# Optimization experiments

Measured on AMD Instinct MI355X. Metric: run time of the kernel, lower is better.

Reference implementation:

```python
import jax, jax.numpy as jnp
import numpy as np

N_NODES = 100000
N_EDGES = 1600000
IN_CH = 128
HID = 128
EMBED = 256
NUM_GRAPHS = 128


def setup_inputs() -> dict:
    key = jax.random.key(0)
    ks = jax.random.split(key, 12)
    x = jax.random.normal(ks[0], (N_NODES, IN_CH), dtype=jnp.float32)
    edge_index = jax.random.randint(ks[1], (2, N_EDGES), 0, N_NODES, dtype=jnp.int64)
    batch = jnp.sort(jax.random.randint(ks[2], (N_NODES,), 0, NUM_GRAPHS, dtype=jnp.int64))
    s = 0.05
    # conv1 MLP: Linear(in_ch,128) -> ReLU -> Linear(128,128)
    W11 = jax.random.normal(ks[3], (IN_CH, HID), dtype=jnp.float32) * s
    b11 = jnp.zeros((HID,), dtype=jnp.float32)
    W12 = jax.random.normal(ks[4], (HID, HID), dtype=jnp.float32) * s
    b12 = jnp.zeros((HID,), dtype=jnp.float32)
    # conv2 MLP: Linear(128,128) -> ReLU -> Linear(128,embed)
    W21 = jax.random.normal(ks[5], (HID, HID), dtype=jnp.float32) * s
    b21 = jnp.zeros((HID,), dtype=jnp.float32)
    W22 = jax.random.normal(ks[6], (HID, EMBED), dtype=jnp.float32) * s
    b22 = jnp.zeros((EMBED,), dtype=jnp.float32)
    gamma = jnp.ones((EMBED,), dtype=jnp.float32)
    beta = jnp.zeros((EMBED,), dtype=jnp.float32)
    return {"x": x, "edge_index": edge_index, "batch": batch,
            "W11": W11, "b11": b11, "W12": W12, "b12": b12,
            "W21": W21, "b21": b21, "W22": W22, "b22": b22,
            "gamma": gamma, "beta": beta}


def _gin_conv(x, src, dst, W_a, b_a, W_b, b_b):
    # GINConv with eps=0: MLP(x + sum_{j in N(i)} x_j)
    msgs = x[src]                                   # [E, d] gather
    agg = jax.ops.segment_sum(msgs, dst, num_segments=N_NODES)  # scatter-add
    h = x + agg
    h = jax.nn.relu(h @ W_a + b_a)
    return h @ W_b + b_b


def reference(x, edge_index, batch, W11, b11, W12, b12, W21, b21, W22, b22, gamma, beta):
    src, dst = edge_index[0], edge_index[1]
    h = jax.nn.relu(_gin_conv(x, src, dst, W11, b11, W12, b12))   # [N, 128]
    h = jax.nn.relu(_gin_conv(h, src, dst, W21, b21, W22, b22))   # [N, 256]
    # global_mean_pool over graphs
    sums = jax.ops.segment_sum(h, batch, num_segments=NUM_GRAPHS)           # [G, 256]
    counts = jax.ops.segment_sum(jnp.ones((N_NODES,), h.dtype), batch, num_segments=NUM_GRAPHS)
    pooled = sums / jnp.maximum(counts, 1.0)[:, None]
    # LayerNorm over last dim (eps=1e-5 as in torch)
    mu = jnp.mean(pooled, axis=-1, keepdims=True)
    var = jnp.var(pooled, axis=-1, keepdims=True)
    out = (pooled - mu) * jax.lax.rsqrt(var + 1e-5) * gamma + beta
    # Dropout in eval mode: identity
    return out
```

## Files before the change

kernel.cpp:

```cpp
#include <hip/hip_runtime.h>

#define GRAPHS 128
#define CHUNKC 4000

typedef _Float16 f16x8 __attribute__((ext_vector_type(8)));
typedef _Float16 f16x4 __attribute__((ext_vector_type(4)));
typedef _Float16 f16x2 __attribute__((ext_vector_type(2)));
typedef float f32x4 __attribute__((ext_vector_type(4)));

__device__ __forceinline__ void fmix_lo(float& a, int w) {
  asm("v_fma_mix_f32 %0, %1, 1.0, %0 op_sel:[0,0,0] op_sel_hi:[1,0,0]" : "+v"(a) : "v"(w));
}
__device__ __forceinline__ void fmix_hi(float& a, int w) {
  asm("v_fma_mix_f32 %0, %1, 1.0, %0 op_sel:[1,0,0] op_sel_hi:[1,0,0]" : "+v"(a) : "v"(w));
}

__global__ void k_prep(const int* __restrict__ dst, int* __restrict__ histG,
                       int e, int NB, int NW,
                       const float* __restrict__ x, _Float16* __restrict__ P0,
                       _Float16* __restrict__ P1, int n,
                       const float* __restrict__ W11, const float* __restrict__ W12,
                       const float* __restrict__ W21, const float* __restrict__ W22,
                       f16x8* __restrict__ f11, f16x8* __restrict__ f12,
                       f16x8* __restrict__ f21, f16x8* __restrict__ f22,
                       float* __restrict__ pool, int cvtb, int wpb, int poolb) {
  __shared__ int h[256];
  int b = blockIdx.x, t = threadIdx.x;
  if (b < NW) {
    h[t] = 0; __syncthreads();
    int lo = b * CHUNKC, hi = min(lo + CHUNKC, e);
    for (int i = lo + t; i < hi; i += 256) atomicAdd(&h[dst[i] >> 9], 1);
    __syncthreads();
    if (t < NB) histG[t * NW + b] = h[t];
    return;
  }
  b -= NW;
  if (b < cvtb) {
    int i = b * 256 + t;
    if (i < n * 32) {
      float4 v = ((const float4*)x)[i];
      f16x4 hh = { (_Float16)v.x, (_Float16)v.y, (_Float16)v.z, (_Float16)v.w };
      ((f16x4*)P0)[i] = hh;
    }
    return;
  }
  b -= cvtb;
  if (b < wpb) {
    int id = b * 256 + t;
    const float* W; f16x8* F; int C, cid, fshift;
    if (id < 2048)       { W = W11; F = f11; C = 128; cid = id;        fshift = 3; }
    else if (id < 4096)  { W = W12; F = f12; C = 128; cid = id - 2048; fshift = 3; }
    else if (id < 6144)  { W = W21; F = f21; C = 128; cid = id - 4096; fshift = 3; }
    else if (id < 10240) { W = W22; F = f22; C = 256; cid = id - 6144; fshift = 4; }
    else return;
    int lane = cid & 63;
    int rest = cid >> 6;
    int fc = rest & ((1 << fshift) - 1);
    int kk = rest >> fshift;
    int cout = fc * 16 + (lane & 15);
    int kb = kk * 32 + (lane >> 4) * 8;
    f16x8 v;
#pragma unroll
    for (int q = 0; q < 8; ++q) v[q] = (_Float16)W[(size_t)(kb + q) * C + cout];
    F[cid] = v;
    return;
  }
  b -= wpb;
  if (b < poolb) {
    int i = b * 256 + t;
    if (i < GRAPHS * 256) pool[i] = 0.f;
    return;
  }
  if (t < 128) P0[(size_t)n * 128 + t] = (_Float16)0.f;
  else P1[(size_t)n * 128 + (t - 128)] = (_Float16)0.f;
}

__global__ void k_scanA(const int* __restrict__ in, int* __restrict__ out,
                        int* __restrict__ bsum, int N) {
  __shared__ int s[256];
  int t = threadIdx.x, b = blockIdx.x;
  int base = b * 1024 + t * 4;
  int v[4]; int tot = 0;
#pragma unroll
  for (int j = 0; j < 4; ++j) { int i = base + j; v[j] = (i < N) ? in[i] : 0; tot += v[j]; }
  s[t] = tot; __syncthreads();
  for (int o = 1; o < 256; o <<= 1) {
    int x = (t >= o) ? s[t - o] : 0;
    __syncthreads(); s[t] += x; __syncthreads();
  }
  int run = s[t] - tot;
#pragma unroll
  for (int j = 0; j < 4; ++j) { int i = base + j; if (i < N) out[i] = run; run += v[j]; }
  if (t == 255) bsum[b] = s[255];
}

__global__ void k_scanB(int* bsum, int nb, const int* __restrict__ batch,
                        int* __restrict__ starts, int n) {
  __shared__ int s[256];
  int t = threadIdx.x;
  int v = (t < nb) ? bsum[t] : 0;
  s[t] = v; __syncthreads();
  for (int o = 1; o < 256; o <<= 1) {
    int x = (t >= o) ? s[t - o] : 0;
    __syncthreads(); s[t] += x; __syncthreads();
  }
  if (t < nb) bsum[t] = s[t] - v;
  if (t <= GRAPHS) {
    int lo = 0, hi = n;
    while (lo < hi) { int mid = (lo + hi) >> 1; if (batch[mid] < t) lo = mid + 1; else hi = mid; }
    starts[t] = lo;
  }
}

__global__ void k_part(const int* __restrict__ src, const int* __restrict__ dst,
                       const int* __restrict__ histG, const int* __restrict__ off,
                       const int* __restrict__ bsum,
                       int* __restrict__ part, int e, int NB, int NW) {
  __shared__ int hist[256], lbA[256], lbB[256], stmp[256];
  __shared__ int els[CHUNKC];
  int t = threadIdx.x, w = blockIdx.x;
  int hv = (t < NB) ? histG[t * NW + w] : 0;
  hist[t] = hv; stmp[t] = hv; __syncthreads();
  for (int o = 1; o < 256; o <<= 1) {
    int x = (t >= o) ? stmp[t - o] : 0;
    __syncthreads(); stmp[t] += x; __syncthreads();
  }
  lbA[t] = stmp[t] - hv; lbB[t] = stmp[t] - hv;
  __syncthreads();
  int lo = w * CHUNKC, hi = min(lo + CHUNKC, e);
  for (int i = lo + t; i < hi; i += 256) {
    int d = dst[i];
    int p = atomicAdd(&lbB[d >> 9], 1);
    els[p] = src[i] | ((d & 511) << 17);
  }
  __syncthreads();
  int ln = t & 63, wv = t >> 6;
  for (int b = wv; b < NB; b += 4) {
    int c = hist[b], lb = lbA[b];
    int idx = b * NW + w;
    long g = off[idx] + bsum[idx >> 10];
    for (int j = ln; j < c; j += 64) part[g + j] = els[lb + j];
  }
}

__global__ void k_csrb(const int* __restrict__ part, const int* __restrict__ off,
                       const int* __restrict__ bsum,
                       int* __restrict__ ptr, int* __restrict__ csr,
                       int e, int NB, int NW, int n) {
  __shared__ int nh[512], ncur[512], stmp[256];
  int t = threadIdx.x, b = blockIdx.x;
  int i0 = b * NW;
  int s0 = off[i0] + bsum[i0 >> 10];
  int e0 = e;
  if (b + 1 < NB) { int i1 = (b + 1) * NW; e0 = off[i1] + bsum[i1 >> 10]; }
  nh[t] = 0; nh[t + 256] = 0; __syncthreads();
  for (int i = s0 + t; i < e0; i += 256) atomicAdd(&nh[((unsigned)part[i]) >> 17], 1);
  __syncthreads();
  int v0 = nh[2 * t], v1 = nh[2 * t + 1];
  int ps = v0 + v1;
  stmp[t] = ps; __syncthreads();
  for (int o = 1; o < 256; o <<= 1) {
    int x = (t >= o) ? stmp[t - o] : 0;
    __syncthreads(); stmp[t] += x; __syncthreads();
  }
  int base = stmp[t] - ps;
  __syncthreads();
  nh[2 * t] = base;   nh[2 * t + 1] = base + v0;
  ncur[2 * t] = base; ncur[2 * t + 1] = base + v0;
  __syncthreads();
#pragma unroll
  for (int q = 0; q < 2; ++q) {
    int vv = t + q * 256;
    int node = (b << 9) + vv;
    if (node <= n) ptr[node] = s0 + nh[vv];
  }
  for (int i = s0 + t; i < e0; i += 256) {
    int u = part[i];
    int p = atomicAdd(&ncur[((unsigned)u) >> 17], 1);
    csr[s0 + p] = u & 0x1FFFF;
  }
}

__global__ void k_agg_h(const _Float16* __restrict__ in, _Float16* __restrict__ out,
                        const int* __restrict__ ptr, const int* __restrict__ csr, int n) {
  int gid = blockIdx.x * 256 + threadIdx.x;
  int node = gid >> 6, lane = gid & 63;
  if (node >= n) return;
  const f16x8* inp = (const f16x8*)in;
  int cb = lane & 15, rg = lane >> 4;
  f16x8 self = inp[(size_t)node * 16 + cb];
  float acc[8];
#pragma unroll
  for (int c = 0; c < 8; ++c) acc[c] = (rg == 0) ? (float)self[c] : 0.f;
  int s = ptr[node], deg = ptr[node + 1] - s;
  union W { f16x8 v; int i[4]; };
  for (int seg = 0; seg < deg; seg += 64) {
    int my = (seg + lane < deg) ? csr[s + seg + lane] : n;
    int segn = min(deg - seg, 64);
    for (int b2 = 0; b2 < segn; b2 += 32) {
      int jj[8]; W w[8];
#pragma unroll
      for (int u = 0; u < 8; ++u) jj[u] = __shfl(my, b2 + u * 4 + rg);
#pragma unroll
      for (int u = 0; u < 8; ++u) w[u].v = inp[(size_t)jj[u] * 16 + cb];
#pragma unroll
      for (int u = 0; u < 8; ++u)
#pragma unroll
        for (int p = 0; p < 4; ++p) {
          fmix_lo(acc[2 * p], w[u].i[p]);
          fmix_hi(acc[2 * p + 1], w[u].i[p]);
        }
    }
  }
#pragma unroll
  for (int c = 0; c < 8; ++c) {
    acc[c] += __shfl_xor(acc[c], 16);
    acc[c] += __shfl_xor(acc[c], 32);
  }
  if (rg == 0) {
    f16x8 r;
#pragma unroll
    for (int c = 0; c < 8; ++c) r[c] = (_Float16)acc[c];
    ((f16x8*)out)[(size_t)node * 16 + cb] = r;
  }
}

__device__ __forceinline__ f16x8 xpose(f32x4 aE, f32x4 aO, int rg) {
  union U2 { _Float16 h[2]; int i; };
  union U8 { int i[4]; f16x8 v; };
  U2 e01, e23, o01, o23;
  e01.h[0] = (_Float16)aE[0]; e01.h[1] = (_Float16)aE[1];
  e23.h[0] = (_Float16)aE[2]; e23.h[1] = (_Float16)aE[3];
  o01.h[0] = (_Float16)aO[0]; o01.h[1] = (_Float16)aO[1];
  o23.h[0] = (_Float16)aO[2]; o23.h[1] = (_Float16)aO[3];
  int e01x1 = __shfl_xor(e01.i, 16), e01x2 = __shfl_xor(e01.i, 32), e01x3 = __shfl_xor(e01.i, 48);
  int e23x1 = __shfl_xor(e23.i, 16), e23x2 = __shfl_xor(e23.i, 32), e23x3 = __shfl_xor(e23.i, 48);
  int o01x1 = __shfl_xor(o01.i, 16), o01x2 = __shfl_xor(o01.i, 32), o01x3 = __shfl_xor(o01.i, 48);
  int o23x1 = __shfl_xor(o23.i, 16), o23x2 = __shfl_xor(o23.i, 32), o23x3 = __shfl_xor(o23.i, 48);
  U8 r;
  r.i[0] = rg == 0 ? e01.i : rg == 1 ? e01x3 : rg == 2 ? o01x2 : o01x1;
  r.i[1] = rg == 0 ? e23.i : rg == 1 ? e23x3 : rg == 2 ? o23x2 : o23x1;
  r.i[2] = rg == 0 ? e01x1 : rg == 1 ? e01x2 : rg == 2 ? o01x3 : o01.i;
  r.i[3] = rg == 0 ? e23x1 : rg == 1 ? e23x2 : rg == 2 ? o23x3 : o23.i;
  return r.v;
}

__launch_bounds__(256, 3)
__global__ void k_mlp128(const _Float16* __restrict__ in, const f16x8* __restrict__ wfA,
                         const float* __restrict__ bA, const f16x8* __restrict__ wfB,
                         const float* __restrict__ bB, _Float16* __restrict__ out, int n) {
  __shared__ f16x8 wf[2048];
  int t = threadIdx.x;
  int r0 = blockIdx.x * 128;
  int lane = t & 63, w = t >> 6;
  int l16 = lane & 15, rg = lane >> 4;
  int rw = w * 32;
  const f16x8* inp = (const f16x8*)in;
#pragma unroll
  for (int i = 0; i < 8; ++i) wf[t + i * 256] = wfA[t + i * 256];
  int ra0 = r0 + rw + l16;      if (ra0 > n) ra0 = n;
  int ra1 = r0 + rw + 16 + l16; if (ra1 > n) ra1 = n;
  f16x8 xf[2][4];
#pragma unroll
  for (int kk = 0; kk < 4; ++kk) {
    xf[0][kk] = inp[(size_t)ra0 * 16 + kk * 4 + rg];
    xf[1][kk] = inp[(size_t)ra1 * 16 + kk * 4 + rg];
  }
  __syncthreads();
  f32x4 acc[2][8];
#pragma unroll
  for (int rs = 0; rs < 2; ++rs)
#pragma unroll
    for (int fc = 0; fc < 8; ++fc) acc[rs][fc] = (f32x4){0.f, 0.f, 0.f, 0.f};
#pragma unroll
  for (int kk = 0; kk < 4; ++kk)
#pragma unroll
    for (int fc = 0; fc < 8; ++fc) {
      f16x8 a = wf[(kk * 8 + fc) * 64 + lane];
      acc[0][fc] = __builtin_amdgcn_mfma_f32_16x16x32_f16(a, xf[0][kk], acc[0][fc], 0, 0, 0);
      acc[1][fc] = __builtin_amdgcn_mfma_f32_16x16x32_f16(a, xf[1][kk], acc[1][fc], 0, 0, 0);
    }
  f16x8 hf[2][4];
#pragma unroll
  for (int fc = 0; fc < 8; ++fc) {
    float4 bv = *(const float4*)(bA + fc * 16 + rg * 4);
#pragma unroll
    for (int rs = 0; rs < 2; ++rs) {
      acc[rs][fc][0] = fmaxf(acc[rs][fc][0] + bv.x, 0.f);
      acc[rs][fc][1] = fmaxf(acc[rs][fc][1] + bv.y, 0.f);
      acc[rs][fc][2] = fmaxf(acc[rs][fc][2] + bv.z, 0.f);
      acc[rs][fc][3] = fmaxf(acc[rs][fc][3] + bv.w, 0.f);
    }
  }
#pragma unroll
  for (int rs = 0; rs < 2; ++rs)
#pragma unroll
    for (int kk = 0; kk < 4; ++kk)
      hf[rs][kk] = xpose(acc[rs][2 * kk], acc[rs][2 * kk + 1], rg);
  __syncthreads();
#pragma unroll
  for (int i = 0; i < 8; ++i) wf[t + i * 256] = wfB[t + i * 256];
  __syncthreads();
#pragma unroll
  for (int rs = 0; rs < 2; ++rs)
#pragma unroll
    for (int fc = 0; fc < 8; ++fc) acc[rs][fc] = (f32x4){0.f, 0.f, 0.f, 0.f};
#pragma unroll
  for (int kk = 0; kk < 4; ++kk)
#pragma unroll
    for (int fc = 0; fc < 8; ++fc) {
      f16x8 b = wf[(kk * 8 + fc) * 64 + lane];
      acc[0][fc] = __builtin_amdgcn_mfma_f32_16x16x32_f16(b, hf[0][kk], acc[0][fc], 0, 0, 0);
      acc[1][fc] = __builtin_amdgcn_mfma_f32_16x16x32_f16(b, hf[1][kk], acc[1][fc], 0, 0, 0);
    }
#pragma unroll
  for (int fc = 0; fc < 8; ++fc) {
    float4 bv = *(const float4*)(bB + fc * 16 + rg * 4);
#pragma unroll
    for (int rs = 0; rs < 2; ++rs) {
      acc[rs][fc][0] = fmaxf(acc[rs][fc][0] + bv.x, 0.f);
      acc[rs][fc][1] = fmaxf(acc[rs][fc][1] + bv.y, 0.f);
      acc[rs][fc][2] = fmaxf(acc[rs][fc][2] + bv.z, 0.f);
      acc[rs][fc][3] = fmaxf(acc[rs][fc][3] + bv.w, 0.f);
    }
  }
  f16x8* outp = (f16x8*)out;
#pragma unroll
  for (int rs = 0; rs < 2; ++rs) {
    int row = r0 + rw + rs * 16 + l16;
#pragma unroll
    for (int kk = 0; kk < 4; ++kk) {
      f16x8 o = xpose(acc[rs][2 * kk], acc[rs][2 * kk + 1], rg);
      if (row < n) outp[(size_t)row * 16 + kk * 4 + rg] = o;
    }
  }
}

__launch_bounds__(256, 3)
__global__ void k_mlp_pool(const _Float16* __restrict__ in, const f16x8* __restrict__ wfA,
                           const float* __restrict__ bA, const f16x8* __restrict__ wfB,
                           const float* __restrict__ bB, const int* __restrict__ batch,
                           float* __restrict__ pool, int n) {
  __shared__ f16x8 wf[2048];
  __shared__ float pool_l[8 * 128];
  int t = threadIdx.x;
  int h = blockIdx.x & 1;
  int r0 = (blockIdx.x >> 1) * 128;
  int lane = t & 63, w = t >> 6;
  int l16 = lane & 15, rg = lane >> 4;
  int rw = w * 32;
  const f16x8* inp = (const f16x8*)in;
#pragma unroll
  for (int j = 0; j < 4; ++j) pool_l[j * 256 + t] = 0.f;
#pragma unroll
  for (int i = 0; i < 8; ++i) wf[t + i * 256] = wfA[t + i * 256];
  int ra0 = r0 + rw + l16;      if (ra0 > n) ra0 = n;
  int ra1 = r0 + rw + 16 + l16; if (ra1 > n) ra1 = n;
  f16x8 xf[2][4];
#pragma unroll
  for (int kk = 0; kk < 4; ++kk) {
    xf[0][kk] = inp[(size_t)ra0 * 16 + kk * 4 + rg];
    xf[1][kk] = inp[(size_t)ra1 * 16 + kk * 4 + rg];
  }
  int g0 = batch[r0];
  int rloc = rw + rg * 4;
  int g4[2][4];
#pragma unroll
  for (int fr = 0; fr < 2; ++fr)
#pragma unroll
    for (int j = 0; j < 4; ++j) {
      int row = r0 + rloc + fr * 16 + j;
      g4[fr][j] = (row < n) ? batch[row] : -1;
    }
  __syncthreads();
  f32x4 acc[2][8];
#pragma unroll
  for (int rs = 0; rs < 2; ++rs)
#pragma unroll
    for (int fc = 0; fc < 8; ++fc) acc[rs][fc] = (f32x4){0.f, 0.f, 0.f, 0.f};
#pragma unroll
  for (int kk = 0; kk < 4; ++kk)
#pragma unroll
    for (int fc = 0; fc < 8; ++fc) {
      f16x8 a = wf[(kk * 8 + fc) * 64 + lane];
      acc[0][fc] = __builtin_amdgcn_mfma_f32_16x16x32_f16(a, xf[0][kk], acc[0][fc], 0, 0, 0);
      acc[1][fc] = __builtin_amdgcn_mfma_f32_16x16x32_f16(a, xf[1][kk], acc[1][fc], 0, 0, 0);
    }
  f16x8 hf[2][4];
#pragma unroll
  for (int fc = 0; fc < 8; ++fc) {
    float4 bv = *(const float4*)(bA + fc * 16 + rg * 4);
#pragma unroll
    for (int rs = 0; rs < 2; ++rs) {
      acc[rs][fc][0] = fmaxf(acc[rs][fc][0] + bv.x, 0.f);
      acc[rs][fc][1] = fmaxf(acc[rs][fc][1] + bv.y, 0.f);
      acc[rs][fc][2] = fmaxf(acc[rs][fc][2] + bv.z, 0.f);
      acc[rs][fc][3] = fmaxf(acc[rs][fc][3] + bv.w, 0.f);
    }
  }
#pragma unroll
  for (int rs = 0; rs < 2; ++rs)
#pragma unroll
    for (int kk = 0; kk < 4; ++kk)
      hf[rs][kk] = xpose(acc[rs][2 * kk], acc[rs][2 * kk + 1], rg);
  __syncthreads();
#pragma unroll
  for (int i = 0; i < 8; ++i) {
    int id = t + i * 256;
    int lj = id & 63, fcl = (id >> 6) & 7, kk = id >> 9;
    wf[id] = wfB[(kk * 16 + h * 8 + fcl) * 64 + lj];
  }
  __syncthreads();
#pragma unroll
  for (int rs = 0; rs < 2; ++rs)
#pragma unroll
    for (int fc = 0; fc < 8; ++fc) acc[rs][fc] = (f32x4){0.f, 0.f, 0.f, 0.f};
#pragma unroll
  for (int kk = 0; kk < 4; ++kk)
#pragma unroll
    for (int fc = 0; fc < 8; ++fc) {
      f16x8 b = wf[(kk * 8 + fc) * 64 + lane];
      acc[0][fc] = __builtin_amdgcn_mfma_f32_16x16x32_f16(hf[0][kk], b, acc[0][fc], 0, 0, 0);
      acc[1][fc] = __builtin_amdgcn_mfma_f32_16x16x32_f16(hf[1][kk], b, acc[1][fc], 0, 0, 0);
    }
#pragma unroll
  for (int fc = 0; fc < 8; ++fc) {
    int col128 = fc * 16 + l16;
    float bv = bB[h * 128 + col128];
#pragma unroll
    for (int fr = 0; fr < 2; ++fr) {
      f32x4 a = acc[fr][fc];
      float run = fmaxf(a[0] + bv, 0.f);
#pragma unroll
      for (int j = 1; j < 4; ++j) {
        float v = fmaxf(a[j] + bv, 0.f);
        if (g4[fr][j] == g4[fr][j - 1]) run += v;
        else {
          int g = g4[fr][j - 1];
          if (g >= 0) {
            int d = g - g0;
            if (d >= 0 && d < 8) atomicAdd(&pool_l[d * 128 + col128], run);
            else atomicAdd(&pool[g * 256 + h * 128 + col128], run);
          }
          run = v;
        }
      }
      int g = g4[fr][3];
      if (g >= 0) {
        int d = g - g0;
        if (d >= 0 && d < 8) atomicAdd(&pool_l[d * 128 + col128], run);
        else atomicAdd(&pool[g * 256 + h * 128 + col128], run);
      }
    }
  }
  __syncthreads();
#pragma unroll
  for (int j = 0; j < 4; ++j) {
    int idx = j * 256 + t;
    int g = g0 + (idx >> 7), col128 = idx & 127;
    float v = pool_l[idx];
    if (g < GRAPHS && v != 0.f) atomicAdd(&pool[g * 256 + h * 128 + col128], v);
  }
}

__global__ void k_final(const float* __restrict__ pool, const int* __restrict__ starts,
                        const float* __restrict__ gamma, const float* __restrict__ beta,
                        float* __restrict__ out) {
  __shared__ float2 red[256];
  int g = blockIdx.x, ch = threadIdx.x;
  int cnt = starts[g + 1] - starts[g];
  float p = pool[g * 256 + ch] / fmaxf((float)cnt, 1.f);
  red[ch] = make_float2(p, p * p);
  __syncthreads();
  for (int off = 128; off > 0; off >>= 1) {
    if (ch < off) { red[ch].x += red[ch + off].x; red[ch].y += red[ch + off].y; }
    __syncthreads();
  }
  float mu = red[0].x * (1.f / 256.f);
  float var = red[0].y * (1.f / 256.f) - mu * mu;
  out[g * 256 + ch] = (p - mu) * rsqrtf(var + 1e-5f) * gamma[ch] + beta[ch];
}

extern "C" void kernel_launch(void* const* d_in, const int* in_sizes, int n_in,
                              void* d_out, int out_size, void* d_ws, size_t ws_size,
                              hipStream_t stream) {
  const float* x     = (const float*)d_in[0];
  const int*   ei    = (const int*)d_in[1];
  const int*   batch = (const int*)d_in[2];
  const float* W11 = (const float*)d_in[3];  const float* b11 = (const float*)d_in[4];
  const float* W12 = (const float*)d_in[5];  const float* b12 = (const float*)d_in[6];
  const float* W21 = (const float*)d_in[7];  const float* b21 = (const float*)d_in[8];
  const float* W22 = (const float*)d_in[9];  const float* b22 = (const float*)d_in[10];
  const float* gamma = (const float*)d_in[11];
  const float* beta  = (const float*)d_in[12];
  float* out = (float*)d_out;

  int n = in_sizes[0] / 128;
  int e = in_sizes[1] / 2;
  const int* src = ei;
  const int* dstv = ei + e;

  int NB = (n + 511) >> 9;
  int NW = (e + CHUNKC - 1) / CHUNKC;
  int NS = NB * NW;

  char* ws = (char*)d_ws;
  auto alloc = [&](size_t bytes) { char* p = ws; ws += (bytes + 15) & ~(size_t)15; return p; };
  _Float16* P0 = (_Float16*)alloc((size_t)(n + 1) * 128 * 2);
  _Float16* P1 = (_Float16*)alloc((size_t)(n + 1) * 128 * 2);
  float* pool  = (float*)alloc((size_t)GRAPHS * 256 * 4);
  int* ptr     = (int*)alloc((size_t)(n + 1) * 4);
  int* csr     = (int*)alloc((size_t)e * 4);
  int* part    = (int*)alloc((size_t)e * 4);
  int* histG   = (int*)alloc((size_t)NS * 4);
  int* off     = (int*)alloc((size_t)NS * 4);
  int* bsum    = (int*)alloc(256 * 4);
  int* starts  = (int*)alloc((GRAPHS + 1) * 4);
  f16x8* f11 = (f16x8*)alloc(2048 * 16);
  f16x8* f12 = (f16x8*)alloc(2048 * 16);
  f16x8* f21 = (f16x8*)alloc(2048 * 16);
  f16x8* f22 = (f16x8*)alloc(4096 * 16);

  int cvtb = (n * 32 + 255) / 256;
  int wpb = 40;
  int poolb = (GRAPHS * 256 + 255) / 256;
  int prepb = NW + cvtb + wpb + poolb + 1;

  int nbk = (NS + 1023) / 1024;
  k_prep <<<prepb, 256, 0, stream>>>(dstv, histG, e, NB, NW, x, P0, P1, n,
                                     W11, W12, W21, W22, f11, f12, f21, f22,
                                     pool, cvtb, wpb, poolb);
  k_scanA<<<nbk, 256, 0, stream>>>(histG, off, bsum, NS);
  k_scanB<<<1, 256, 0, stream>>>(bsum, nbk, batch, starts, n);
  k_part <<<NW, 256, 0, stream>>>(src, dstv, histG, off, bsum, part, e, NB, NW);
  k_csrb <<<NB, 256, 0, stream>>>(part, off, bsum, ptr, csr, e, NB, NW, n);

  int mb = (n + 127) / 128;
  int ab = (n * 64 + 255) / 256;

  k_agg_h<<<ab, 256, 0, stream>>>(P0, P1, ptr, csr, n);
  k_mlp128<<<mb, 256, 0, stream>>>(P1, f11, b11, f12, b12, P0, n);
  k_agg_h<<<ab, 256, 0, stream>>>(P0, P1, ptr, csr, n);
  k_mlp_pool<<<mb * 2, 256, 0, stream>>>(P1, f21, b21, f22, b22, batch, pool, n);
  k_final<<<GRAPHS, 256, 0, stream>>>(pool, starts, gamma, beta, out);
}
```

Before: 276.9 us.

## Replace global pool atomics with per-block partials reduced in final kernel

Shared-memory pooling accumulators are replicated four ways, indexed by row group, so lanes no longer contend on the same LDS address. Each block writes its local per-graph partial sums to a global scratch buffer instead of issuing global atomics. The final LayerNorm kernel then sums the relevant tile partials per graph. This removes most global atomic traffic at the cost of 4x LDS for pool_l, which may reduce occupancy, and a serial tile loop in k_final.

Measured after the change: 282.7 us. 1.02x slower.

```diff
diff --git a/kernel.cpp b/kernel.cpp
--- a/kernel.cpp
+++ b/kernel.cpp
@@ -340,9 +340,9 @@
 __global__ void k_mlp_pool(const _Float16* __restrict__ in, const f16x8* __restrict__ wfA,
                            const float* __restrict__ bA, const f16x8* __restrict__ wfB,
                            const float* __restrict__ bB, const int* __restrict__ batch,
-                           float* __restrict__ pool, int n) {
+                           float* __restrict__ pool, float* __restrict__ scratch, int n) {
   __shared__ f16x8 wf[2048];
-  __shared__ float pool_l[8 * 128];
+  __shared__ float pool_l[8 * 128 * 4];
   int t = threadIdx.x;
   int h = blockIdx.x & 1;
   int r0 = (blockIdx.x >> 1) * 128;
@@ -351,7 +351,7 @@
   int rw = w * 32;
   const f16x8* inp = (const f16x8*)in;
 #pragma unroll
-  for (int j = 0; j < 4; ++j) pool_l[j * 256 + t] = 0.f;
+  for (int j = 0; j < 16; ++j) pool_l[j * 256 + t] = 0.f;
 #pragma unroll
   for (int i = 0; i < 8; ++i) wf[t + i * 256] = wfA[t + i * 256];
   int ra0 = r0 + rw + l16;      if (ra0 > n) ra0 = n;
@@ -439,7 +439,7 @@
           int g = g4[fr][j - 1];
           if (g >= 0) {
             int d = g - g0;
-            if (d >= 0 && d < 8) atomicAdd(&pool_l[d * 128 + col128], run);
+            if (d >= 0 && d < 8) atomicAdd(&pool_l[(d * 128 + col128) * 4 + rg], run);
             else atomicAdd(&pool[g * 256 + h * 128 + col128], run);
           }
           run = v;
@@ -448,28 +448,40 @@
       int g = g4[fr][3];
       if (g >= 0) {
         int d = g - g0;
-        if (d >= 0 && d < 8) atomicAdd(&pool_l[d * 128 + col128], run);
+        if (d >= 0 && d < 8) atomicAdd(&pool_l[(d * 128 + col128) * 4 + rg], run);
         else atomicAdd(&pool[g * 256 + h * 128 + col128], run);
       }
     }
   }
   __syncthreads();
+  float* sb = scratch + (size_t)blockIdx.x * 1024;
 #pragma unroll
   for (int j = 0; j < 4; ++j) {
     int idx = j * 256 + t;
-    int g = g0 + (idx >> 7), col128 = idx & 127;
-    float v = pool_l[idx];
-    if (g < GRAPHS && v != 0.f) atomicAdd(&pool[g * 256 + h * 128 + col128], v);
-  }
-}
-
-__global__ void k_final(const float* __restrict__ pool, const int* __restrict__ starts,
+    float4 v4 = *(const float4*)&pool_l[idx * 4];
+    sb[idx] = (v4.x + v4.y) + (v4.z + v4.w);
+  }
+}
+
+__global__ void k_final(const float* __restrict__ scratch, const float* __restrict__ pool,
+                        const int* __restrict__ starts, const int* __restrict__ batch,
                         const float* __restrict__ gamma, const float* __restrict__ beta,
                         float* __restrict__ out) {
   __shared__ float2 red[256];
   int g = blockIdx.x, ch = threadIdx.x;
-  int cnt = starts[g + 1] - starts[g];
-  float p = pool[g * 256 + ch] / fmaxf((float)cnt, 1.f);
+  int h = ch >> 7, c = ch & 127;
+  int s0 = starts[g], s1 = starts[g + 1];
+  float p = pool[g * 256 + ch];
+  if (s1 > s0) {
+    int t0 = s0 >> 7, t1 = (s1 - 1) >> 7;
+    for (int tile = t0; tile <= t1; ++tile) {
+      int d = g - batch[tile << 7];
+      if (d >= 0 && d < 8)
+        p += scratch[(size_t)((tile << 1) | h) * 1024 + d * 128 + c];
+    }
+  }
+  int cnt = s1 - s0;
+  p /= fmaxf((float)cnt, 1.f);
   red[ch] = make_float2(p, p * p);
   __syncthreads();
   for (int off = 128; off > 0; off >>= 1) {
@@ -503,12 +515,14 @@
   int NB = (n + 511) >> 9;
   int NW = (e + CHUNKC - 1) / CHUNKC;
   int NS = NB * NW;
+  int mb = (n + 127) / 128;
 
   char* ws = (char*)d_ws;
   auto alloc = [&](size_t bytes) { char* p = ws; ws += (bytes + 15) & ~(size_t)15; return p; };
   _Float16* P0 = (_Float16*)alloc((size_t)(n + 1) * 128 * 2);
   _Float16* P1 = (_Float16*)alloc((size_t)(n + 1) * 128 * 2);
   float* pool  = (float*)alloc((size_t)GRAPHS * 256 * 4);
+  float* scratch = (float*)alloc((size_t)mb * 2 * 1024 * 4);
   int* ptr     = (int*)alloc((size_t)(n + 1) * 4);
   int* csr     = (int*)alloc((size_t)e * 4);
   int* part    = (int*)alloc((size_t)e * 4);
@@ -535,12 +549,11 @@
   k_part <<<NW, 256, 0, stream>>>(src, dstv, histG, off, bsum, part, e, NB, NW);
   k_csrb <<<NB, 256, 0, stream>>>(part, off, bsum, ptr, csr, e, NB, NW, n);
 
-  int mb = (n + 127) / 128;
   int ab = (n * 64 + 255) / 256;
 
   k_agg_h<<<ab, 256, 0, stream>>>(P0, P1, ptr, csr, n);
   k_mlp128<<<mb, 256, 0, stream>>>(P1, f11, b11, f12, b12, P0, n);
   k_agg_h<<<ab, 256, 0, stream>>>(P0, P1, ptr, csr, n);
-  k_mlp_pool<<<mb * 2, 256, 0, stream>>>(P1, f21, b21, f22, b22, batch, pool, n);
-  k_final<<<GRAPHS, 256, 0, stream>>>(pool, starts, gamma, beta, out);
-}
+  k_mlp_pool<<<mb * 2, 256, 0, stream>>>(P1, f21, b21, f22, b22, batch, pool, scratch, n);
+  k_final<<<GRAPHS, 256, 0, stream>>>(scratch, pool, starts, batch, gamma, beta, out);
+}
```
